# Performance work log

Hardware: AMD Instinct MI355X
Metric: run time of the kernel (lower is better)

The kernel has to match this reference:

```python
import jax, jax.numpy as jnp
import numpy as np
from jax import lax

THRESH = 0.6      # pnet score threshold (threshold[0])
IOU_THR = 0.5     # per-scale nms threshold in detect_face
K_PICKS = 128     # fixed max number of NMS picks (jit-static)
STRIDE = 2.0
CELL = 12.0
NEG = -1e30


def _conv(x, w, b):
    y = lax.conv_general_dilated(x, w, (1, 1), 'VALID',
                                 dimension_numbers=('NCHW', 'OIHW', 'NCHW'))
    return y + b[None, :, None, None]


def _prelu(x, a):
    return jnp.where(x > 0, x, a[None, :, None, None] * x)


def _maxpool2(x):
    return lax.reduce_window(x, -jnp.inf, lax.max, (1, 1, 2, 2), (1, 1, 2, 2), 'VALID')


def _nms(boxes, scores):
    # Greedy union-IoU NMS (nms_numpy math), vectorized with a fixed pick budget.
    # boxes [N,4] (shared grid), scores [N] with invalid entries already = NEG.
    x1, y1, x2, y2 = boxes[:, 0], boxes[:, 1], boxes[:, 2], boxes[:, 3]
    area = (x2 - x1 + 1.0) * (y2 - y1 + 1.0)

    def body(live, _):
        j = jnp.argmax(live)
        s = live[j]
        ok = s > NEG * 0.5
        xx1 = jnp.maximum(x1[j], x1); yy1 = jnp.maximum(y1[j], y1)
        xx2 = jnp.minimum(x2[j], x2); yy2 = jnp.minimum(y2[j], y2)
        inter = jnp.maximum(0.0, xx2 - xx1 + 1.0) * jnp.maximum(0.0, yy2 - yy1 + 1.0)
        iou = inter / (area[j] + area - inter)
        live = jnp.where(iou > IOU_THR, NEG, live).at[j].set(NEG)
        return live, (j, ok)

    _, (idx, ok) = lax.scan(body, scores, None, length=K_PICKS)
    return idx, ok


def setup_inputs():
    key = jax.random.key(0)
    ks = jax.random.split(key, 16)
    B, H, W = 16, 384, 512
    f = lambda k, shp, s=0.1: jax.random.normal(k, shp, jnp.float32) * s
    return {
        'im_data': jax.random.uniform(ks[0], (B, 3, H, W), jnp.float32) * 255.0,
        'c1_w': f(ks[1], (10, 3, 3, 3)), 'c1_b': f(ks[2], (10,)),
        'p1': jnp.full((10,), 0.25, jnp.float32),
        'c2_w': f(ks[3], (16, 10, 3, 3)), 'c2_b': f(ks[4], (16,)),
        'p2': jnp.full((16,), 0.25, jnp.float32),
        'c3_w': f(ks[5], (32, 16, 3, 3)), 'c3_b': f(ks[6], (32,)),
        'p3': jnp.full((32,), 0.25, jnp.float32),
        'c41_w': f(ks[7], (2, 32, 1, 1)), 'c41_b': f(ks[8], (2,)),
        'c42_w': f(ks[9], (4, 32, 1, 1)), 'c42_b': f(ks[10], (4,)),
    }


def reference(im_data, c1_w, c1_b, p1, c2_w, c2_b, p2, c3_w, c3_b, p3,
              c41_w, c41_b, c42_w, c42_b):
    # --- PNet conv trunk (detect_face normalization + MTCNN PNet) ---
    x = (im_data - 127.5) * 0.0078125
    h = _prelu(_conv(x, c1_w, c1_b), p1)
    h = _maxpool2(h)                                   # 2x2 s2 (dims even -> ceil==floor)
    h = _prelu(_conv(h, c2_w, c2_b), p2)
    h = _prelu(_conv(h, c3_w, c3_b), p3)
    probs = jax.nn.softmax(_conv(h, c41_w, c41_b), axis=1)[:, 1]   # [B,Hp,Wp]
    reg = _conv(h, c42_w, c42_b)                                   # [B,4,Hp,Wp]

    # --- generateBoundingBox (dense, masked instead of nonzero; scale=1) ---
    B, Hp, Wp = probs.shape
    yy, xx = jnp.meshgrid(jnp.arange(Hp, dtype=jnp.float32),
                          jnp.arange(Wp, dtype=jnp.float32), indexing='ij')
    boxes4 = jnp.stack([jnp.floor(STRIDE * xx + 1.0).ravel(),
                        jnp.floor(STRIDE * yy + 1.0).ravel(),
                        jnp.floor(STRIDE * xx + CELL).ravel(),
                        jnp.floor(STRIDE * yy + CELL).ravel()], axis=1)  # [N,4]
    scores = probs.reshape(B, -1)                                   # [B,N]
    regf = reg.reshape(B, 4, -1).transpose(0, 2, 1)                 # [B,N,4]
    masked = jnp.where(scores >= THRESH, scores, NEG)

    # --- per-image greedy NMS (batched_nms: images independent) ---
    idx, ok = jax.vmap(_nms, in_axes=(None, 0))(boxes4, masked)     # [B,K]
    pb = boxes4[idx]                                                # [B,K,4]
    ps = jnp.take_along_axis(scores, idx, axis=1)                   # [B,K]
    pr = jnp.take_along_axis(regf, idx[..., None], axis=1)          # [B,K,4]

    w = pb[..., 2] - pb[..., 0]
    hh = pb[..., 3] - pb[..., 1]
    q1 = pb[..., 0] + pr[..., 0] * w
    q2 = pb[..., 1] + pr[..., 1] * hh
    q3 = pb[..., 2] + pr[..., 2] * w
    q4 = pb[..., 3] + pr[..., 3] * hh
    rw = q3 - q1
    rh = q4 - q2
    l = jnp.maximum(rw, rh)
    nx1 = q1 + rw * 0.5 - l * 0.5
    ny1 = q2 + rh * 0.5 - l * 0.5
    out = jnp.stack([nx1, ny1, nx1 + l, ny1 + l, ps], axis=-1)      # [B,K,5]
    return out * ok[..., None].astype(out.dtype)
```

## Files before the change

kernel.cpp:

```cpp
#include <hip/hip_runtime.h>
#include <math.h>

#define BATCH 16
#define IH 384
#define IW 512
#define C1 10
#define P1H 191
#define P1W 255
#define C2 16
#define H2 189
#define W2 253
#define C3 32
#define H3 187
#define W3 251
#define N3 (H3*W3)
#define KP 128
#define CAP 7680
#define NEGV (-1e30f)

__global__ __launch_bounds__(256, 2) void k_conv1pool(
        const float* __restrict__ im, const float* __restrict__ w,
        const float* __restrict__ bia, const float* __restrict__ slope,
        float* __restrict__ outp) {
    int x = blockIdx.x * 16 + threadIdx.x;
    int y = blockIdx.y * 16 + threadIdx.y;
    int bb = blockIdx.z;
    if (x >= P1W || y >= P1H) return;

    float in[3][4][4];
    #pragma unroll
    for (int ci = 0; ci < 3; ++ci) {
        const float* p = im + (((size_t)bb * 3 + ci) * IH + 2 * y) * IW + 2 * x;
        #pragma unroll
        for (int r = 0; r < 4; ++r) {
            const float2* q = (const float2*)(p + (size_t)r * IW);
            float2 a0 = q[0], a1 = q[1];
            in[ci][r][0] = a0.x; in[ci][r][1] = a0.y;
            in[ci][r][2] = a1.x; in[ci][r][3] = a1.y;
        }
    }
    #pragma unroll
    for (int ci = 0; ci < 3; ++ci)
        #pragma unroll
        for (int r = 0; r < 4; ++r)
            #pragma unroll
            for (int c = 0; c < 4; ++c)
                in[ci][r][c] = (in[ci][r][c] - 127.5f) * 0.0078125f;

    #pragma unroll
    for (int oc = 0; oc < C1; ++oc) {
        const float* wo = w + oc * 27;
        float bv = bia[oc], sv = slope[oc];
        float best = -INFINITY;
        #pragma unroll
        for (int py = 0; py < 2; ++py)
            #pragma unroll
            for (int px = 0; px < 2; ++px) {
                float acc = bv;
                #pragma unroll
                for (int ci = 0; ci < 3; ++ci)
                    #pragma unroll
                    for (int ky = 0; ky < 3; ++ky)
                        #pragma unroll
                        for (int kx = 0; kx < 3; ++kx)
                            acc += in[ci][py + ky][px + kx] * wo[(ci * 3 + ky) * 3 + kx];
                float v = acc > 0.f ? acc : sv * acc;
                best = fmaxf(best, v);
            }
        outp[(((size_t)bb * C1 + oc) * P1H + y) * P1W + x] = best;
    }
}

__global__ __launch_bounds__(256, 2) void k_conv2(
        const float* __restrict__ inp, const float* __restrict__ w,
        const float* __restrict__ bia, const float* __restrict__ slope,
        float* __restrict__ outp) {
    int x0 = (blockIdx.x * 64 + threadIdx.x) * 2;
    int y  = blockIdx.y * 4 + threadIdx.y;
    int bb = blockIdx.z;
    if (x0 >= W2 || y >= H2) return;

    float a0[C2], a1[C2];
    #pragma unroll
    for (int oc = 0; oc < C2; ++oc) { a0[oc] = bia[oc]; a1[oc] = bia[oc]; }

    bool tail = (x0 + 3 > P1W - 1);

    for (int ci = 0; ci < C1; ++ci) {
        const float* p = inp + (((size_t)bb * C1 + ci) * P1H + y) * P1W + x0;
        float v[3][4];
        #pragma unroll
        for (int r = 0; r < 3; ++r) {
            const float* pr = p + (size_t)r * P1W;
            v[r][0] = pr[0]; v[r][1] = pr[1]; v[r][2] = pr[2];
            v[r][3] = tail ? 0.f : pr[3];
        }
        const float* wc = w + ci * 9;
        #pragma unroll
        for (int oc = 0; oc < C2; ++oc) {
            const float* wo = wc + oc * (C1 * 9);
            float s0 = a0[oc], s1 = a1[oc];
            #pragma unroll
            for (int ky = 0; ky < 3; ++ky)
                #pragma unroll
                for (int kx = 0; kx < 3; ++kx) {
                    float wv = wo[ky * 3 + kx];
                    s0 += v[ky][kx]     * wv;
                    s1 += v[ky][kx + 1] * wv;
                }
            a0[oc] = s0; a1[oc] = s1;
        }
    }
    bool px1 = (x0 + 1 < W2);
    #pragma unroll
    for (int oc = 0; oc < C2; ++oc) {
        float sl = slope[oc];
        float* o = outp + (((size_t)bb * C2 + oc) * H2 + y) * W2 + x0;
        float u0 = a0[oc]; o[0] = u0 > 0.f ? u0 : sl * u0;
        if (px1) { float u1 = a1[oc]; o[1] = u1 > 0.f ? u1 : sl * u1; }
    }
}

__global__ __launch_bounds__(256, 2) void k_conv3heads(
        const float* __restrict__ inp, const float* __restrict__ w3,
        const float* __restrict__ b3, const float* __restrict__ s3,
        const float* __restrict__ w41, const float* __restrict__ b41,
        const float* __restrict__ w42, const float* __restrict__ b42,
        float* __restrict__ scores, float4* __restrict__ regf) {
    int x0 = (blockIdx.x * 64 + threadIdx.x) * 2;
    int y  = blockIdx.y * 4 + threadIdx.y;
    int bb = blockIdx.z;
    if (x0 >= W3 || y >= H3) return;

    float a0[C3], a1[C3];
    #pragma unroll
    for (int oc = 0; oc < C3; ++oc) { a0[oc] = b3[oc]; a1[oc] = b3[oc]; }

    bool tail = (x0 + 3 > W2 - 1);

    for (int ci = 0; ci < C2; ++ci) {
        const float* p = inp + (((size_t)bb * C2 + ci) * H2 + y) * W2 + x0;
        float v[3][4];
        #pragma unroll
        for (int r = 0; r < 3; ++r) {
            const float* pr = p + (size_t)r * W2;
            v[r][0] = pr[0]; v[r][1] = pr[1]; v[r][2] = pr[2];
            v[r][3] = tail ? 0.f : pr[3];
        }
        const float* wc = w3 + ci * 9;
        #pragma unroll
        for (int oc = 0; oc < C3; ++oc) {
            const float* wo = wc + oc * (C2 * 9);
            float s0 = a0[oc], s1 = a1[oc];
            #pragma unroll
            for (int ky = 0; ky < 3; ++ky)
                #pragma unroll
                for (int kx = 0; kx < 3; ++kx) {
                    float wv = wo[ky * 3 + kx];
                    s0 += v[ky][kx]     * wv;
                    s1 += v[ky][kx + 1] * wv;
                }
            a0[oc] = s0; a1[oc] = s1;
        }
    }
    #pragma unroll
    for (int oc = 0; oc < C3; ++oc) {
        float u0 = a0[oc], u1 = a1[oc], sl = s3[oc];
        a0[oc] = u0 > 0.f ? u0 : sl * u0;
        a1[oc] = u1 > 0.f ? u1 : sl * u1;
    }

    float l00 = b41[0], l01 = b41[1], l10 = b41[0], l11 = b41[1];
    #pragma unroll
    for (int c = 0; c < C3; ++c) {
        float w0 = w41[c], w1 = w41[C3 + c];
        l00 += a0[c] * w0; l01 += a0[c] * w1;
        l10 += a1[c] * w0; l11 += a1[c] * w1;
    }
    float m0 = fmaxf(l00, l01), m1 = fmaxf(l10, l11);
    float p0 = expf(l01 - m0) / (expf(l00 - m0) + expf(l01 - m0));
    float p1 = expf(l11 - m1) / (expf(l10 - m1) + expf(l11 - m1));

    float r00 = b42[0], r01 = b42[1], r02 = b42[2], r03 = b42[3];
    float r10 = b42[0], r11 = b42[1], r12 = b42[2], r13 = b42[3];
    #pragma unroll
    for (int c = 0; c < C3; ++c) {
        float w0 = w42[c], w1 = w42[C3 + c], w2 = w42[2 * C3 + c], w3v = w42[3 * C3 + c];
        r00 += a0[c] * w0; r01 += a0[c] * w1; r02 += a0[c] * w2; r03 += a0[c] * w3v;
        r10 += a1[c] * w0; r11 += a1[c] * w1; r12 += a1[c] * w2; r13 += a1[c] * w3v;
    }

    size_t n0 = (size_t)bb * N3 + y * W3 + x0;
    scores[n0] = (p0 >= 0.6f) ? p0 : NEGV;
    regf[n0]   = make_float4(r00, r01, r02, r03);
    if (x0 + 1 < W3) {
        scores[n0 + 1] = (p1 >= 0.6f) ? p1 : NEGV;
        regf[n0 + 1]   = make_float4(r10, r11, r12, r13);
    }
}

__global__ __launch_bounds__(1024) void k_nms(
        const float* __restrict__ scores, const float4* __restrict__ regf,
        float* __restrict__ outp) {
    __shared__ float s_score[CAP];
    __shared__ int   s_idx[CAP];
    __shared__ float r_s[16];
    __shared__ int   r_i[16];
    __shared__ float s_picks[KP];
    __shared__ int   s_picki[KP];
    __shared__ int   s_misc[4];

    int tid = threadIdx.x;
    int bb = blockIdx.x;
    const float* sc = scores + (size_t)bb * N3;

    if (tid < 4) s_misc[tid] = 0;
    __syncthreads();

    int cnt = 0;
    for (int i = tid; i < N3; i += 1024) if (sc[i] > 0.f) cnt++;
    atomicAdd(&s_misc[0], cnt);
    __syncthreads();
    int M = s_misc[0];

    int cutbin = 0;
    if (M > CAP) {
        for (int i = tid; i < 2048; i += 1024) s_idx[i] = 0;
        __syncthreads();
        for (int i = tid; i < N3; i += 1024) {
            float s = sc[i];
            if (s > 0.f) {
                int b = (int)((s - 0.6f) * 5120.f);
                b = b < 0 ? 0 : (b > 2047 ? 2047 : b);
                atomicAdd(&s_idx[b], 1);
            }
        }
        __syncthreads();
        if (tid == 0) {
            int accum = 0, b = 2047;
            for (; b >= 0; --b) {
                int c = s_idx[b];
                if (accum + c > CAP) break;
                accum += c;
            }
            s_misc[2] = b + 1;
        }
        __syncthreads();
        cutbin = s_misc[2];
        __syncthreads();
    }

    for (int i = tid; i < N3; i += 1024) {
        float s = sc[i];
        if (s > 0.f) {
            bool keep = true;
            if (M > CAP) {
                int b = (int)((s - 0.6f) * 5120.f);
                b = b < 0 ? 0 : (b > 2047 ? 2047 : b);
                keep = (b >= cutbin);
            }
            if (keep) {
                int pos = atomicAdd(&s_misc[1], 1);
                if (pos < CAP) { s_score[pos] = s; s_idx[pos] = i; }
            }
        }
    }
    __syncthreads();
    int M2 = s_misc[1]; if (M2 > CAP) M2 = CAP;

    int np = 0;
    for (int pick = 0; pick < KP; ++pick) {
        float bs = -INFINITY; int bi = 0x7fffffff;
        for (int i = tid; i < M2; i += 1024) {
            float s = s_score[i]; int id = s_idx[i];
            if (s > bs || (s == bs && id < bi)) { bs = s; bi = id; }
        }
        #pragma unroll
        for (int off = 32; off; off >>= 1) {
            float os = __shfl_down(bs, off);
            int   oi = __shfl_down(bi, off);
            if (os > bs || (os == bs && oi < bi)) { bs = os; bi = oi; }
        }
        int lane = tid & 63, wv = tid >> 6;
        if (lane == 0) { r_s[wv] = bs; r_i[wv] = bi; }
        __syncthreads();
        if (tid == 0) {
            float ps = r_s[0]; int pi = r_i[0];
            for (int k = 1; k < 16; ++k) {
                float os = r_s[k]; int oi = r_i[k];
                if (os > ps || (os == ps && oi < pi)) { ps = os; pi = oi; }
            }
            s_picks[pick] = ps; s_picki[pick] = pi;
            r_s[0] = ps; r_i[0] = pi;
        }
        __syncthreads();
        float ps = r_s[0]; int pi = r_i[0];
        if (ps < 0.f) break;
        np = pick + 1;

        int pcx = pi % W3, pcy = pi / W3;
        float px1 = (float)(2 * pcx + 1), py1 = (float)(2 * pcy + 1);
        float px2 = (float)(2 * pcx + 12), py2 = (float)(2 * pcy + 12);
        for (int i = tid; i < M2; i += 1024) {
            float s = s_score[i];
            if (s > NEGV * 0.5f) {
                int id = s_idx[i];
                int cx = id % W3, cy = id / W3;
                float x1 = (float)(2 * cx + 1), y1 = (float)(2 * cy + 1);
                float x2 = (float)(2 * cx + 12), y2 = (float)(2 * cy + 12);
                float xx1 = fmaxf(px1, x1), yy1 = fmaxf(py1, y1);
                float xx2 = fminf(px2, x2), yy2 = fminf(py2, y2);
                float inter = fmaxf(0.f, xx2 - xx1 + 1.f) * fmaxf(0.f, yy2 - yy1 + 1.f);
                float iou = inter / (288.f - inter);
                if (iou > 0.5f) s_score[i] = NEGV;
            }
        }
        __syncthreads();
    }

    if (tid < KP) {
        float* o = outp + ((size_t)bb * KP + tid) * 5;
        if (tid < np) {
            int pi = s_picki[tid]; float ps = s_picks[tid];
            int cx = pi % W3, cy = pi / W3;
            float x1 = (float)(2 * cx + 1), y1 = (float)(2 * cy + 1);
            float x2 = (float)(2 * cx + 12), y2 = (float)(2 * cy + 12);
            float4 r = regf[(size_t)bb * N3 + pi];
            float wd = x2 - x1, hh = y2 - y1;
            float q1 = x1 + r.x * wd, q2 = y1 + r.y * hh;
            float q3 = x2 + r.z * wd, q4 = y2 + r.w * hh;
            float rw = q3 - q1, rh = q4 - q2;
            float L = fmaxf(rw, rh);
            float nx1 = q1 + rw * 0.5f - L * 0.5f;
            float ny1 = q2 + rh * 0.5f - L * 0.5f;
            o[0] = nx1; o[1] = ny1; o[2] = nx1 + L; o[3] = ny1 + L; o[4] = ps;
        } else {
            o[0] = 0.f; o[1] = 0.f; o[2] = 0.f; o[3] = 0.f; o[4] = 0.f;
        }
    }
}

extern "C" void kernel_launch(void* const* d_in, const int* in_sizes, int n_in,
                              void* d_out, int out_size, void* d_ws, size_t ws_size,
                              hipStream_t stream) {
    const float* im   = (const float*)d_in[0];
    const float* c1w  = (const float*)d_in[1];
    const float* c1b  = (const float*)d_in[2];
    const float* p1   = (const float*)d_in[3];
    const float* c2w  = (const float*)d_in[4];
    const float* c2b  = (const float*)d_in[5];
    const float* p2   = (const float*)d_in[6];
    const float* c3w  = (const float*)d_in[7];
    const float* c3b  = (const float*)d_in[8];
    const float* p3   = (const float*)d_in[9];
    const float* c41w = (const float*)d_in[10];
    const float* c41b = (const float*)d_in[11];
    const float* c42w = (const float*)d_in[12];
    const float* c42b = (const float*)d_in[13];

    float* ws = (float*)d_ws;
    const size_t POOL1_FLOATS = (size_t)BATCH * C1 * P1H * P1W;
    float*  pool1  = ws;
    float*  conv2b = ws + POOL1_FLOATS;
    float*  scoresb = ws;
    float4* regfb   = (float4*)(ws + (size_t)BATCH * N3);

    k_conv1pool<<<dim3(16, 12, BATCH), dim3(16, 16), 0, stream>>>(im, c1w, c1b, p1, pool1);
    k_conv2   <<<dim3(2, 48, BATCH), dim3(64, 4), 0, stream>>>(pool1, c2w, c2b, p2, conv2b);
    k_conv3heads<<<dim3(2, 47, BATCH), dim3(64, 4), 0, stream>>>(conv2b, c3w, c3b, p3,
                                                                 c41w, c41b, c42w, c42b,
                                                                 scoresb, regfb);
    k_nms<<<dim3(BATCH), dim3(1024), 0, stream>>>(scoresb, regfb, (float*)d_out);
}
```

Baseline: 267.9 us.

## Rewrite NMS as single-wave top-K register scan; reshape conv blocks and repack conv3 weights

Result: slower. 294.5 us (+9.9%).

```diff
diff --git a/kernel.cpp b/kernel.cpp
--- a/kernel.cpp
+++ b/kernel.cpp
@@ -15,17 +15,17 @@
 #define W3 251
 #define N3 (H3*W3)
 #define KP 128
-#define CAP 7680
+#define NCAP 1536
 #define NEGV (-1e30f)
 
-__global__ __launch_bounds__(256, 2) void k_conv1pool(
+__global__ __launch_bounds__(64, 2) void k_conv1pool(
         const float* __restrict__ im, const float* __restrict__ w,
         const float* __restrict__ bia, const float* __restrict__ slope,
         float* __restrict__ outp) {
-    int x = blockIdx.x * 16 + threadIdx.x;
-    int y = blockIdx.y * 16 + threadIdx.y;
+    int x = blockIdx.x * 64 + threadIdx.x;
+    int y = blockIdx.y;
     int bb = blockIdx.z;
-    if (x >= P1W || y >= P1H) return;
+    if (x >= P1W) return;
 
     float in[3][4][4];
     #pragma unroll
@@ -71,14 +71,14 @@
     }
 }
 
-__global__ __launch_bounds__(256, 2) void k_conv2(
+__global__ __launch_bounds__(64, 2) void k_conv2(
         const float* __restrict__ inp, const float* __restrict__ w,
         const float* __restrict__ bia, const float* __restrict__ slope,
         float* __restrict__ outp) {
     int x0 = (blockIdx.x * 64 + threadIdx.x) * 2;
-    int y  = blockIdx.y * 4 + threadIdx.y;
+    int y  = blockIdx.y;
     int bb = blockIdx.z;
-    if (x0 >= W2 || y >= H2) return;
+    if (x0 >= W2) return;
 
     float a0[C2], a1[C2];
     #pragma unroll
@@ -121,16 +121,25 @@
     }
 }
 
-__global__ __launch_bounds__(256, 2) void k_conv3heads(
-        const float* __restrict__ inp, const float* __restrict__ w3,
+__global__ void k_repack(const float* __restrict__ w3, float* __restrict__ w3t) {
+    int i = blockIdx.x * 256 + threadIdx.x;
+    if (i < C3 * C2 * 9) {
+        int k = i % 9, r = i / 9;
+        int ci = r / C3, oc = r % C3;
+        w3t[i] = w3[(oc * C2 + ci) * 9 + k];
+    }
+}
+
+__global__ __launch_bounds__(64, 2) void k_conv3heads(
+        const float* __restrict__ inp, const float* __restrict__ w3t,
         const float* __restrict__ b3, const float* __restrict__ s3,
         const float* __restrict__ w41, const float* __restrict__ b41,
         const float* __restrict__ w42, const float* __restrict__ b42,
         float* __restrict__ scores, float4* __restrict__ regf) {
     int x0 = (blockIdx.x * 64 + threadIdx.x) * 2;
-    int y  = blockIdx.y * 4 + threadIdx.y;
+    int y  = blockIdx.y;
     int bb = blockIdx.z;
-    if (x0 >= W3 || y >= H3) return;
+    if (x0 >= W3) return;
 
     float a0[C3], a1[C3];
     #pragma unroll
@@ -147,10 +156,10 @@
             v[r][0] = pr[0]; v[r][1] = pr[1]; v[r][2] = pr[2];
             v[r][3] = tail ? 0.f : pr[3];
         }
-        const float* wc = w3 + ci * 9;
+        const float* wc = w3t + ci * (C3 * 9);
         #pragma unroll
         for (int oc = 0; oc < C3; ++oc) {
-            const float* wo = wc + oc * (C2 * 9);
+            const float* wo = wc + oc * 9;
             float s0 = a0[oc], s1 = a1[oc];
             #pragma unroll
             for (int ky = 0; ky < 3; ++ky)
@@ -190,7 +199,7 @@
         r10 += a1[c] * w0; r11 += a1[c] * w1; r12 += a1[c] * w2; r13 += a1[c] * w3v;
     }
 
-    size_t n0 = (size_t)bb * N3 + y * W3 + x0;
+    size_t n0 = (size_t)bb * N3 + (size_t)y * W3 + x0;
     scores[n0] = (p0 >= 0.6f) ? p0 : NEGV;
     regf[n0]   = make_float4(r00, r01, r02, r03);
     if (x0 + 1 < W3) {
@@ -202,138 +211,127 @@
 __global__ __launch_bounds__(1024) void k_nms(
         const float* __restrict__ scores, const float4* __restrict__ regf,
         float* __restrict__ outp) {
-    __shared__ float s_score[CAP];
-    __shared__ int   s_idx[CAP];
-    __shared__ float r_s[16];
-    __shared__ int   r_i[16];
-    __shared__ float s_picks[KP];
-    __shared__ int   s_picki[KP];
-    __shared__ int   s_misc[4];
+    __shared__ int   hist[2048];
+    __shared__ float cs[NCAP];
+    __shared__ int   cc[NCAP];
+    __shared__ float psk[KP];
+    __shared__ int   pck[KP];
+    __shared__ int   misc[2];
 
     int tid = threadIdx.x;
     int bb = blockIdx.x;
     const float* sc = scores + (size_t)bb * N3;
 
-    if (tid < 4) s_misc[tid] = 0;
+    for (int i = tid; i < 2048; i += 1024) hist[i] = 0;
+    if (tid < 2) misc[tid] = 0;
     __syncthreads();
-
-    int cnt = 0;
-    for (int i = tid; i < N3; i += 1024) if (sc[i] > 0.f) cnt++;
-    atomicAdd(&s_misc[0], cnt);
-    __syncthreads();
-    int M = s_misc[0];
-
-    int cutbin = 0;
-    if (M > CAP) {
-        for (int i = tid; i < 2048; i += 1024) s_idx[i] = 0;
-        __syncthreads();
-        for (int i = tid; i < N3; i += 1024) {
-            float s = sc[i];
-            if (s > 0.f) {
-                int b = (int)((s - 0.6f) * 5120.f);
-                b = b < 0 ? 0 : (b > 2047 ? 2047 : b);
-                atomicAdd(&s_idx[b], 1);
-            }
-        }
-        __syncthreads();
-        if (tid == 0) {
-            int accum = 0, b = 2047;
-            for (; b >= 0; --b) {
-                int c = s_idx[b];
-                if (accum + c > CAP) break;
-                accum += c;
-            }
-            s_misc[2] = b + 1;
-        }
-        __syncthreads();
-        cutbin = s_misc[2];
-        __syncthreads();
-    }
 
     for (int i = tid; i < N3; i += 1024) {
         float s = sc[i];
         if (s > 0.f) {
-            bool keep = true;
-            if (M > CAP) {
-                int b = (int)((s - 0.6f) * 5120.f);
-                b = b < 0 ? 0 : (b > 2047 ? 2047 : b);
-                keep = (b >= cutbin);
+            int b = (int)((s - 0.6f) * 5120.f);
+            b = b < 0 ? 0 : (b > 2047 ? 2047 : b);
+            atomicAdd(&hist[b], 1);
+        }
+    }
+    __syncthreads();
+
+    if (tid < 64) {
+        int part = 0;
+        #pragma unroll 8
+        for (int k = 0; k < 32; ++k) part += hist[tid * 32 + k];
+        int suf = part;
+        #pragma unroll
+        for (int off = 1; off < 64; off <<= 1) {
+            int o = __shfl_down(suf, off);
+            suf += (tid + off < 64) ? o : 0;
+        }
+        int M = __shfl(suf, 0);
+        int target = M < 1152 ? M : 1152;
+        int base = suf - part;
+        if (M > 0 && base < target && base + part >= target) {
+            int acc = base, cb = tid * 32;
+            for (int b = tid * 32 + 31; b >= tid * 32; --b) {
+                acc += hist[b];
+                if (acc >= target) { cb = b; break; }
             }
-            if (keep) {
-                int pos = atomicAdd(&s_misc[1], 1);
-                if (pos < CAP) { s_score[pos] = s; s_idx[pos] = i; }
+            misc[1] = cb;
+        }
+    }
+    __syncthreads();
+    int cutbin = misc[1];
+
+    for (int i = tid; i < N3; i += 1024) {
+        float s = sc[i];
+        if (s > 0.f) {
+            int b = (int)((s - 0.6f) * 5120.f);
+            b = b < 0 ? 0 : (b > 2047 ? 2047 : b);
+            if (b >= cutbin) {
+                int pos = atomicAdd(&misc[0], 1);
+                if (pos < NCAP) {
+                    int cy = i / W3, cx = i - cy * W3;
+                    cs[pos] = s;
+                    cc[pos] = (cy << 16) | cx;
+                }
             }
         }
     }
     __syncthreads();
-    int M2 = s_misc[1]; if (M2 > CAP) M2 = CAP;
-
-    int np = 0;
-    for (int pick = 0; pick < KP; ++pick) {
-        float bs = -INFINITY; int bi = 0x7fffffff;
-        for (int i = tid; i < M2; i += 1024) {
-            float s = s_score[i]; int id = s_idx[i];
-            if (s > bs || (s == bs && id < bi)) { bs = s; bi = id; }
+    if (tid >= 64) return;
+
+    int K = misc[0]; if (K > NCAP) K = NCAP;
+    K = __builtin_amdgcn_readfirstlane(K);
+    int lane = tid;
+
+    float sreg[24]; int cxr[24], cyr[24];
+    #pragma unroll
+    for (int j = 0; j < 24; ++j) {
+        int e = j * 64 + lane;
+        bool v = e < K;
+        float s = v ? cs[e] : -INFINITY;
+        int c = v ? cc[e] : 0x7FFF7FFF;
+        sreg[j] = s; cxr[j] = c & 0xffff; cyr[j] = c >> 16;
+    }
+
+    int np = 0, ppx = -10000, ppy = -10000;
+    for (int t = 0; t < KP; ++t) {
+        float bs = -INFINITY; int bc = 0x7FFFFFFF;
+        #pragma unroll
+        for (int j = 0; j < 24; ++j) {
+            if (j * 64 < K) {
+                if ((unsigned)(cxr[j] - ppx + 1) <= 2u &&
+                    (unsigned)(cyr[j] - ppy + 1) <= 2u) sreg[j] = -INFINITY;
+                float s = sreg[j]; int c = (cyr[j] << 16) | cxr[j];
+                if (s > bs || (s == bs && c < bc)) { bs = s; bc = c; }
+            }
         }
         #pragma unroll
         for (int off = 32; off; off >>= 1) {
-            float os = __shfl_down(bs, off);
-            int   oi = __shfl_down(bi, off);
-            if (os > bs || (os == bs && oi < bi)) { bs = os; bi = oi; }
-        }
-        int lane = tid & 63, wv = tid >> 6;
-        if (lane == 0) { r_s[wv] = bs; r_i[wv] = bi; }
-        __syncthreads();
-        if (tid == 0) {
-            float ps = r_s[0]; int pi = r_i[0];
-            for (int k = 1; k < 16; ++k) {
-                float os = r_s[k]; int oi = r_i[k];
-                if (os > ps || (os == ps && oi < pi)) { ps = os; pi = oi; }
-            }
-            s_picks[pick] = ps; s_picki[pick] = pi;
-            r_s[0] = ps; r_i[0] = pi;
-        }
-        __syncthreads();
-        float ps = r_s[0]; int pi = r_i[0];
-        if (ps < 0.f) break;
-        np = pick + 1;
-
-        int pcx = pi % W3, pcy = pi / W3;
-        float px1 = (float)(2 * pcx + 1), py1 = (float)(2 * pcy + 1);
-        float px2 = (float)(2 * pcx + 12), py2 = (float)(2 * pcy + 12);
-        for (int i = tid; i < M2; i += 1024) {
-            float s = s_score[i];
-            if (s > NEGV * 0.5f) {
-                int id = s_idx[i];
-                int cx = id % W3, cy = id / W3;
-                float x1 = (float)(2 * cx + 1), y1 = (float)(2 * cy + 1);
-                float x2 = (float)(2 * cx + 12), y2 = (float)(2 * cy + 12);
-                float xx1 = fmaxf(px1, x1), yy1 = fmaxf(py1, y1);
-                float xx2 = fminf(px2, x2), yy2 = fminf(py2, y2);
-                float inter = fmaxf(0.f, xx2 - xx1 + 1.f) * fmaxf(0.f, yy2 - yy1 + 1.f);
-                float iou = inter / (288.f - inter);
-                if (iou > 0.5f) s_score[i] = NEGV;
-            }
-        }
-        __syncthreads();
-    }
-
-    if (tid < KP) {
-        float* o = outp + ((size_t)bb * KP + tid) * 5;
-        if (tid < np) {
-            int pi = s_picki[tid]; float ps = s_picks[tid];
-            int cx = pi % W3, cy = pi / W3;
-            float x1 = (float)(2 * cx + 1), y1 = (float)(2 * cy + 1);
+            float os = __shfl_xor(bs, off);
+            int   oc_ = __shfl_xor(bc, off);
+            if (os > bs || (os == bs && oc_ < bc)) { bs = os; bc = oc_; }
+        }
+        if (bs < 0.f) break;
+        if (lane == 0) { psk[t] = bs; pck[t] = bc; }
+        np = t + 1;
+        ppx = bc & 0xffff; ppy = bc >> 16;
+    }
+
+    for (int t = lane; t < KP; t += 64) {
+        float* o = outp + ((size_t)bb * KP + t) * 5;
+        if (t < np) {
+            int c = pck[t]; float s = psk[t];
+            int cx = c & 0xffff, cy = c >> 16;
+            float x1 = (float)(2 * cx + 1),  y1 = (float)(2 * cy + 1);
             float x2 = (float)(2 * cx + 12), y2 = (float)(2 * cy + 12);
-            float4 r = regf[(size_t)bb * N3 + pi];
-            float wd = x2 - x1, hh = y2 - y1;
-            float q1 = x1 + r.x * wd, q2 = y1 + r.y * hh;
-            float q3 = x2 + r.z * wd, q4 = y2 + r.w * hh;
+            float4 r = regf[(size_t)bb * N3 + (size_t)cy * W3 + cx];
+            float q1 = x1 + r.x * 11.f, q2 = y1 + r.y * 11.f;
+            float q3 = x2 + r.z * 11.f, q4 = y2 + r.w * 11.f;
             float rw = q3 - q1, rh = q4 - q2;
             float L = fmaxf(rw, rh);
             float nx1 = q1 + rw * 0.5f - L * 0.5f;
             float ny1 = q2 + rh * 0.5f - L * 0.5f;
-            o[0] = nx1; o[1] = ny1; o[2] = nx1 + L; o[3] = ny1 + L; o[4] = ps;
+            o[0] = nx1; o[1] = ny1; o[2] = nx1 + L; o[3] = ny1 + L; o[4] = s;
         } else {
             o[0] = 0.f; o[1] = 0.f; o[2] = 0.f; o[3] = 0.f; o[4] = 0.f;
         }
@@ -360,15 +358,17 @@
 
     float* ws = (float*)d_ws;
     const size_t POOL1_FLOATS = (size_t)BATCH * C1 * P1H * P1W;
-    float*  pool1  = ws;
-    float*  conv2b = ws + POOL1_FLOATS;
+    float*  pool1   = ws;
+    float*  conv2b  = ws + POOL1_FLOATS;
     float*  scoresb = ws;
     float4* regfb   = (float4*)(ws + (size_t)BATCH * N3);
-
-    k_conv1pool<<<dim3(16, 12, BATCH), dim3(16, 16), 0, stream>>>(im, c1w, c1b, p1, pool1);
-    k_conv2   <<<dim3(2, 48, BATCH), dim3(64, 4), 0, stream>>>(pool1, c2w, c2b, p2, conv2b);
-    k_conv3heads<<<dim3(2, 47, BATCH), dim3(64, 4), 0, stream>>>(conv2b, c3w, c3b, p3,
-                                                                 c41w, c41b, c42w, c42b,
-                                                                 scoresb, regfb);
+    float*  w3t     = ws + 4000000;
+
+    k_conv1pool<<<dim3(4, P1H, BATCH), dim3(64), 0, stream>>>(im, c1w, c1b, p1, pool1);
+    k_conv2   <<<dim3(2, H2, BATCH), dim3(64), 0, stream>>>(pool1, c2w, c2b, p2, conv2b);
+    k_repack  <<<dim3(18), dim3(256), 0, stream>>>(c3w, w3t);
+    k_conv3heads<<<dim3(2, H3, BATCH), dim3(64), 0, stream>>>(conv2b, w3t, c3b, p3,
+                                                              c41w, c41b, c42w, c42b,
+                                                              scoresb, regfb);
     k_nms<<<dim3(BATCH), dim3(1024), 0, stream>>>(scoresb, regfb, (float*)d_out);
 }
```
